# Kernel optimization log

Hardware: AMD Instinct MI355X
Metric: run time of the kernel (lower is better)

## Reference

```python
import jax, jax.numpy as jnp
import numpy as np

B, DC, DB, DF = 16384, 2048, 768, 256
NF = DB  # num_features (isSwinT=True)
EPS = 1e-5


def setup_inputs() -> dict:
    key = jax.random.key(0)
    ks = jax.random.split(key, 20)
    s = 0.02
    return {
        'x_context': jax.random.normal(ks[0], (B, DC), jnp.float32),
        'x_body': jax.random.normal(ks[1], (B, DB), jnp.float32),
        'x_face': jax.random.normal(ks[2], (B, DF), jnp.float32),
        'Wc': jax.random.normal(ks[3], (NF, DC), jnp.float32) * s,
        'bc': jax.random.normal(ks[4], (NF,), jnp.float32) * s,
        'Wa1': jax.random.normal(ks[5], (128, NF), jnp.float32) * s,
        'ba1': jax.random.normal(ks[6], (128,), jnp.float32) * s,
        'ga': jnp.ones((128,), jnp.float32),
        'bba': jnp.zeros((128,), jnp.float32),
        'Wa2': jax.random.normal(ks[7], (1, 128), jnp.float32) * s,
        'ba2': jax.random.normal(ks[8], (1,), jnp.float32) * s,
        'W1': jax.random.normal(ks[9], (256, NF * 3), jnp.float32) * s,
        'b1': jax.random.normal(ks[10], (256,), jnp.float32) * s,
        'g1': jnp.ones((256,), jnp.float32),
        'be1': jnp.zeros((256,), jnp.float32),
        'Wcat': jax.random.normal(ks[11], (26, 256), jnp.float32) * s,
        'bcat': jax.random.normal(ks[12], (26,), jnp.float32) * s,
    }


def _bn(x, g, b):
    # BatchNorm1d, training mode (biased batch stats), deterministic
    m = jnp.mean(x, axis=0)
    v = jnp.mean((x - m) ** 2, axis=0)
    return (x - m) * jax.lax.rsqrt(v + EPS) * g + b


def reference(x_context, x_body, x_face, Wc, bc, Wa1, ba1, ga, bba, Wa2, ba2,
              W1, b1, g1, be1, Wcat, bcat):
    # face repeated elementwise to body width: [B,256,1]->repeat(3)->view[B,768]
    face = jnp.repeat(x_face, DB // DF, axis=1)              # [B, NF]
    ctx = x_context @ Wc.T + bc                              # [B, NF]
    body = x_body                                            # [B, NF]

    def cross_atten(a, u, v):
        # two 1x1 dot-products, softmax over size-2 dim, weighted sum
        d = jnp.stack([jnp.sum(a * u, axis=1), jnp.sum(a * v, axis=1)], axis=1)  # [B,2]
        att = jax.nn.softmax(d, axis=1)
        # sum over dim2 of a[:, :, None] @ att[:, None, :] == a * att.sum(1)
        return a * jnp.sum(att, axis=1, keepdims=True)

    cfeat = cross_atten(ctx, body, face)
    bfeat = cross_atten(body, ctx, face)
    ffeat = cross_atten(face, ctx, body)

    def fc_att(x):
        h = _bn(x @ Wa1.T + ba1, ga, bba)
        h = jax.nn.gelu(h, approximate=False)
        return h @ Wa2.T + ba2                               # [B, 1]

    score = jax.nn.softmax(
        jnp.concatenate([fc_att(cfeat), fc_att(bfeat), fc_att(ffeat)], axis=1), axis=1)  # [B,3]
    cfeat = cfeat * score[:, 0:1]
    bfeat = bfeat * score[:, 1:2]
    ffeat = ffeat * score[:, 2:3]

    fuse = jnp.concatenate([cfeat, bfeat, ffeat], axis=1) @ W1.T + b1  # [B,256]
    fuse = jax.nn.relu(_bn(fuse, g1, be1))  # dropout p=0.5 treated as identity (eval)
    return fuse @ Wcat.T + bcat             # [B,26]
```

## Files before the change

### kernel.cpp

```cpp
#include <hip/hip_runtime.h>
#include <hip/hip_bf16.h>
#include <stdint.h>

typedef float f32x4 __attribute__((ext_vector_type(4)));
typedef short bf16x8 __attribute__((ext_vector_type(8)));
typedef unsigned short u16;

static constexpr int kB  = 16384;
static constexpr int kDC = 2048;
static constexpr int kNF = 768;
static constexpr float kEps = 1e-5f;

static constexpr size_t OFF_FEATS  = 0;
static constexpr size_t OFF_X      = 75497472;
static constexpr size_t OFF_WCBF   = OFF_X + 67108864;
static constexpr size_t OFF_WA1BF  = OFF_WCBF + 3145728;
static constexpr size_t OFF_W1BF   = OFF_WA1BF + 196608;
static constexpr size_t OFF_FUSE   = OFF_W1BF + 1179648;
static constexpr size_t OFF_SCORES = OFF_FUSE + 16777216;
static constexpr size_t OFF_STATS  = OFF_SCORES + 196608;

static __device__ __forceinline__ u16 f2bf(float x) {
  union { float f; unsigned u; } c; c.f = x;
  unsigned r = c.u + 0x7fffu + ((c.u >> 16) & 1u);
  return (u16)(r >> 16);
}

static __device__ __forceinline__ void cvt8x4(const float* __restrict__ in,
                                              u16* __restrict__ out, long base) {
  float4 f[8];
#pragma unroll
  for (int i = 0; i < 8; ++i) f[i] = ((const float4*)in)[base + i * 256];
#pragma unroll
  for (int i = 0; i < 8; ++i)
    ((ushort4*)out)[base + i * 256] =
        make_ushort4(f2bf(f[i].x), f2bf(f[i].y), f2bf(f[i].z), f2bf(f[i].w));
}

__global__ __launch_bounds__(256) void prep_kernel(
    const float* __restrict__ xc, const float* __restrict__ Wc,
    const float* __restrict__ Wa1, const float* __restrict__ W1,
    u16* __restrict__ axbf, u16* __restrict__ wcbf,
    u16* __restrict__ wa1bf, u16* __restrict__ w1bf)
{
  const int b = blockIdx.x, t = threadIdx.x;
  const float* in; u16* out; long base;
  if (b < 4096)      { in = xc;  out = axbf;  base = (long)b * 2048 + t; }
  else if (b < 4288) { in = Wc;  out = wcbf;  base = (long)(b - 4096) * 2048 + t; }
  else if (b < 4300) { in = Wa1; out = wa1bf; base = (long)(b - 4288) * 2048 + t; }
  else               { in = W1;  out = w1bf;  base = (long)(b - 4300) * 2048 + t; }
  cvt8x4(in, out, base);
}

static __device__ __forceinline__ void gload16(const void* g, void* l) {
  __builtin_amdgcn_global_load_lds(
      (const __attribute__((address_space(1))) void*)g,
      (__attribute__((address_space(3))) void*)l, 16, 0, 0);
}

__global__ __launch_bounds__(256) void gemm_ctx_conv(
    const u16* __restrict__ A, const u16* __restrict__ B,
    const float* __restrict__ bias, u16* __restrict__ C,
    const float* __restrict__ xb, const float* __restrict__ xf,
    u16* __restrict__ feats)
{
  __shared__ __align__(16) u16 As[128 * 32];
  __shared__ __align__(16) u16 Bs[128 * 32];
  const int id = blockIdx.x, t = threadIdx.x;

  if (id >= 768) {
    const int c = id - 768;
    if (c < 1536) {
      cvt8x4(xb, feats + (size_t)kB * kNF, (long)c * 2048 + t);
    } else {
      const long base = (long)(c - 1536) * 2048 + t;
      float4 f[8];
#pragma unroll
      for (int i = 0; i < 8; ++i) f[i] = ((const float4*)xf)[base + i * 256];
#pragma unroll
      for (int i = 0; i < 8; ++i) {
        const long v = base + i * 256;
        u16 e0 = f2bf(f[i].x), e1 = f2bf(f[i].y), e2 = f2bf(f[i].z), e3 = f2bf(f[i].w);
        size_t p = (size_t)v * 4;
        size_t row = p >> 8;
        int col = (int)(p & 255);
        u16* o = feats + (size_t)2 * kB * kNF + row * kNF + col * 3;
        ushort4* o4 = (ushort4*)o;
        o4[0] = make_ushort4(e0, e0, e0, e1);
        o4[1] = make_ushort4(e1, e1, e2, e2);
        o4[2] = make_ushort4(e2, e3, e3, e3);
      }
    }
    return;
  }

  const int bx = id & 127, by = id >> 7;
  const size_t m0 = (size_t)bx * 128;
  const int n0 = by * 128;
  const int lane = t & 63, wave = t >> 6;
  const int wm = (wave >> 1) * 64, wn = (wave & 1) * 64;
  const int fr = lane & 15, fq = lane >> 4;

  const int srow = t >> 2, scol = (t & 3) * 8;
  const u16* ga0 = A + (m0 + srow) * (size_t)kDC + scol;
  const u16* ga1 = A + (m0 + 64 + srow) * (size_t)kDC + scol;
  const u16* gb0 = B + (size_t)(n0 + srow) * kDC + scol;
  const u16* gb1 = B + (size_t)(n0 + 64 + srow) * kDC + scol;
  u16* la = As + t * 8;
  u16* lb = Bs + t * 8;
  const u16* fa = As + (wm + fr) * 32 + fq * 8;
  const u16* fb = Bs + (wn + fr) * 32 + fq * 8;

  f32x4 acc[4][4] = {};

  for (int k = 0; k < 64; ++k) {
    __syncthreads();
    gload16(ga0, la);
    gload16(ga1, la + 2048);
    gload16(gb0, lb);
    gload16(gb1, lb + 2048);
    ga0 += 32; ga1 += 32; gb0 += 32; gb1 += 32;
    __syncthreads();
    bf16x8 av[4], bv[4];
#pragma unroll
    for (int mf = 0; mf < 4; ++mf) av[mf] = *(const bf16x8*)(fa + mf * 512);
#pragma unroll
    for (int nf = 0; nf < 4; ++nf) bv[nf] = *(const bf16x8*)(fb + nf * 512);
#pragma unroll
    for (int mf = 0; mf < 4; ++mf)
#pragma unroll
      for (int nf = 0; nf < 4; ++nf)
        acc[mf][nf] = __builtin_amdgcn_mfma_f32_16x16x32_bf16(av[mf], bv[nf], acc[mf][nf], 0, 0, 0);
  }

#pragma unroll
  for (int mf = 0; mf < 4; ++mf) {
    const size_t rb = m0 + wm + mf * 16 + fq * 4;
#pragma unroll
    for (int nf = 0; nf < 4; ++nf) {
      const int gn = n0 + wn + nf * 16 + fr;
      const float bb = bias[gn];
#pragma unroll
      for (int rr = 0; rr < 4; ++rr)
        C[(rb + rr) * (size_t)kNF + gn] = f2bf(acc[mf][nf][rr] + bb);
    }
  }
}

template <int STATS>
__global__ __launch_bounds__(256) void gemm_bt64(
    const u16* __restrict__ A, int lda, const u16* __restrict__ B, int ldb,
    const float* __restrict__ bias, float* __restrict__ C, int ldc, int K,
    float* __restrict__ stats)
{
  __shared__ __align__(16) u16 As[2 * 64 * 32];
  __shared__ __align__(16) u16 Bs[2 * 128 * 32];
  const int bx = blockIdx.x, by = blockIdx.y;
  const size_t m0 = (size_t)bx * 64;
  const int n0 = by * 128;
  const int t = threadIdx.x;
  const int lane = t & 63, wave = t >> 6;
  const int wn = wave * 32;
  const int fr = lane & 15, fq = lane >> 4;

  const int srow = t >> 2, scol = (t & 3) * 8;
  const u16* ga0 = A + (m0 + srow) * (size_t)lda + scol;
  const u16* gb0 = B + (size_t)(n0 + srow) * ldb + scol;
  const u16* gb1 = B + (size_t)(n0 + 64 + srow) * ldb + scol;

  f32x4 acc[4][2] = {};

  gload16(ga0, As + t * 8);
  gload16(gb0, Bs + t * 8);
  gload16(gb1, Bs + t * 8 + 2048);
  ga0 += 32; gb0 += 32; gb1 += 32;
  __syncthreads();

  const int kt = K >> 5;
  for (int k = 0; k < kt; ++k) {
    const int cur = k & 1;
    if (k + 1 < kt) {
      u16* an = As + (cur ^ 1) * 2048;
      u16* bn = Bs + (cur ^ 1) * 4096;
      gload16(ga0, an + t * 8);
      gload16(gb0, bn + t * 8);
      gload16(gb1, bn + t * 8 + 2048);
      ga0 += 32; gb0 += 32; gb1 += 32;
    }
    const u16* fa = As + cur * 2048 + fr * 32 + fq * 8;
    const u16* fb = Bs + cur * 4096 + (wn + fr) * 32 + fq * 8;
    bf16x8 av[4], bv[2];
#pragma unroll
    for (int mf = 0; mf < 4; ++mf) av[mf] = *(const bf16x8*)(fa + mf * 512);
#pragma unroll
    for (int nf = 0; nf < 2; ++nf) bv[nf] = *(const bf16x8*)(fb + nf * 512);
#pragma unroll
    for (int mf = 0; mf < 4; ++mf)
#pragma unroll
      for (int nf = 0; nf < 2; ++nf)
        acc[mf][nf] = __builtin_amdgcn_mfma_f32_16x16x32_bf16(av[mf], bv[nf], acc[mf][nf], 0, 0, 0);
    __syncthreads();
  }

  float cs[2] = {}, cs2[2] = {};
#pragma unroll
  for (int mf = 0; mf < 4; ++mf) {
    const size_t rb = m0 + mf * 16 + fq * 4;
#pragma unroll
    for (int nf = 0; nf < 2; ++nf) {
      const int gn = n0 + wn + nf * 16 + fr;
      const float bb = bias[gn];
#pragma unroll
      for (int rr = 0; rr < 4; ++rr) {
        const float vv = acc[mf][nf][rr] + bb;
        C[(rb + rr) * (size_t)ldc + gn] = vv;
        if (STATS) { cs[nf] += vv; cs2[nf] += vv * vv; }
      }
    }
  }
  if (STATS) {
    const int f = (int)(m0 >> 14);
#pragma unroll
    for (int nf = 0; nf < 2; ++nf) {
      float s = cs[nf], s2 = cs2[nf];
      s += __shfl_down(s, 32); s2 += __shfl_down(s2, 32);
      s += __shfl_down(s, 16); s2 += __shfl_down(s2, 16);
      if (fq == 0) {
        const int gn = n0 + wn + nf * 16 + fr;
        atomicAdd(&stats[(f * 128 + gn) * 2 + 0], s);
        atomicAdd(&stats[(f * 128 + gn) * 2 + 1], s2);
      }
    }
  }
}

__global__ __launch_bounds__(256) void gemm_fuse64(
    const u16* __restrict__ feats, const u16* __restrict__ w1,
    const float* __restrict__ scores, const float* __restrict__ b1,
    float* __restrict__ fuse, float* __restrict__ fstats)
{
  __shared__ __align__(16) u16 As[2 * 64 * 32];
  __shared__ __align__(16) u16 Bs[2 * 128 * 32];
  const int bx = blockIdx.x, by = blockIdx.y;
  const size_t m0 = (size_t)bx * 64;
  const int n0 = by * 128;
  const int t = threadIdx.x;
  const int lane = t & 63, wave = t >> 6;
  const int wn = wave * 32;
  const int fr = lane & 15, fq = lane >> 4;
  const int srow = t >> 2, scol = (t & 3) * 8;

  const u16* ga0; const u16* gb0; const u16* gb1;
  auto setf = [&](int f) {
    ga0 = feats + (size_t)f * kB * kNF + (m0 + srow) * (size_t)kNF + scol;
    gb0 = w1 + f * kNF + (size_t)(n0 + srow) * 2304 + scol;
    gb1 = gb0 + (size_t)64 * 2304;
  };

  const f32x4 vzero = {};
  f32x4 acc[4][2] = {}, tot[4][2] = {};

  setf(0);
  gload16(ga0, As + t * 8);
  gload16(gb0, Bs + t * 8);
  gload16(gb1, Bs + t * 8 + 2048);
  ga0 += 32; gb0 += 32; gb1 += 32;
  int pf = 0, pk = 1;
  int ck = 0, cf = 0;
  __syncthreads();

  for (int s = 0; s < 72; ++s) {
    const int cur = s & 1;
    if (s < 71) {
      u16* an = As + (cur ^ 1) * 2048;
      u16* bn = Bs + (cur ^ 1) * 4096;
      gload16(ga0, an + t * 8);
      gload16(gb0, bn + t * 8);
      gload16(gb1, bn + t * 8 + 2048);
      if (++pk == 24) { pk = 0; ++pf; if (pf < 3) setf(pf); }
      else { ga0 += 32; gb0 += 32; gb1 += 32; }
    }
    const u16* fa = As + cur * 2048 + fr * 32 + fq * 8;
    const u16* fb = Bs + cur * 4096 + (wn + fr) * 32 + fq * 8;
    bf16x8 av[4], bv[2];
#pragma unroll
    for (int mf = 0; mf < 4; ++mf) av[mf] = *(const bf16x8*)(fa + mf * 512);
#pragma unroll
    for (int nf = 0; nf < 2; ++nf) bv[nf] = *(const bf16x8*)(fb + nf * 512);
#pragma unroll
    for (int mf = 0; mf < 4; ++mf)
#pragma unroll
      for (int nf = 0; nf < 2; ++nf)
        acc[mf][nf] = __builtin_amdgcn_mfma_f32_16x16x32_bf16(av[mf], bv[nf], acc[mf][nf], 0, 0, 0);
    if (++ck == 24) {
      ck = 0;
#pragma unroll
      for (int mf = 0; mf < 4; ++mf) {
        const size_t rb = m0 + mf * 16 + fq * 4;
#pragma unroll
        for (int rr = 0; rr < 4; ++rr) {
          const float sv = scores[(rb + rr) * 3 + cf];
#pragma unroll
          for (int nf = 0; nf < 2; ++nf) tot[mf][nf][rr] += sv * acc[mf][nf][rr];
        }
      }
#pragma unroll
      for (int mf = 0; mf < 4; ++mf)
#pragma unroll
        for (int nf = 0; nf < 2; ++nf) acc[mf][nf] = vzero;
      ++cf;
    }
    __syncthreads();
  }

  float cs[2] = {}, cs2[2] = {};
#pragma unroll
  for (int mf = 0; mf < 4; ++mf) {
    const size_t rb = m0 + mf * 16 + fq * 4;
#pragma unroll
    for (int nf = 0; nf < 2; ++nf) {
      const int gn = n0 + wn + nf * 16 + fr;
      const float bb = b1[gn];
#pragma unroll
      for (int rr = 0; rr < 4; ++rr) {
        const float vv = tot[mf][nf][rr] + bb;
        fuse[(rb + rr) * 256 + gn] = vv;
        cs[nf] += vv; cs2[nf] += vv * vv;
      }
    }
  }
#pragma unroll
  for (int nf = 0; nf < 2; ++nf) {
    float s = cs[nf], s2 = cs2[nf];
    s += __shfl_down(s, 32); s2 += __shfl_down(s2, 32);
    s += __shfl_down(s, 16); s2 += __shfl_down(s2, 16);
    if (fq == 0) {
      const int gn = n0 + wn + nf * 16 + fr;
      atomicAdd(&fstats[gn * 2 + 0], s);
      atomicAdd(&fstats[gn * 2 + 1], s2);
    }
  }
}

__global__ __launch_bounds__(64) void att_kernel(
    const float* __restrict__ H, const float* __restrict__ stats,
    const float* __restrict__ ga, const float* __restrict__ bba,
    const float* __restrict__ Wa2, const float* __restrict__ ba2,
    float* __restrict__ scores)
{
  const int i = blockIdx.x, l = threadIdx.x;
  float d[3];
#pragma unroll
  for (int f = 0; f < 3; ++f) {
    float part = 0.f;
#pragma unroll
    for (int h = 0; h < 2; ++h) {
      const int c = l + h * 64;
      const float sum = stats[(f * 128 + c) * 2 + 0];
      const float sq  = stats[(f * 128 + c) * 2 + 1];
      const float m = sum * (1.f / kB);
      const float var = sq * (1.f / kB) - m * m;
      const float rs = rsqrtf(var + kEps);
      const float x = H[((size_t)f * kB + i) * 128 + c];
      const float xn = (x - m) * rs * ga[c] + bba[c];
      const float ge = 0.5f * xn * (1.f + erff(xn * 0.70710678118f));
      part += ge * Wa2[c];
    }
#pragma unroll
    for (int off = 32; off > 0; off >>= 1) part += __shfl_down(part, off);
    d[f] = part;
  }
  if (l == 0) {
    const float b2 = ba2[0];
    float d0 = d[0] + b2, d1 = d[1] + b2, d2 = d[2] + b2;
    const float mx = fmaxf(d0, fmaxf(d1, d2));
    const float e0 = expf(d0 - mx), e1 = expf(d1 - mx), e2 = expf(d2 - mx);
    const float inv = 1.f / (e0 + e1 + e2);
    scores[i * 3 + 0] = e0 * inv;
    scores[i * 3 + 1] = e1 * inv;
    scores[i * 3 + 2] = e2 * inv;
  }
}

__global__ __launch_bounds__(64) void final_kernel(
    const float* __restrict__ fuse, const float* __restrict__ fstats,
    const float* __restrict__ g1, const float* __restrict__ be1,
    const float* __restrict__ Wcat, const float* __restrict__ bcat,
    float* __restrict__ out)
{
  const int i = blockIdx.x, l = threadIdx.x;
  __shared__ float row[256];
#pragma unroll
  for (int h = 0; h < 4; ++h) {
    const int c = l + h * 64;
    const float sum = fstats[c * 2 + 0], sq = fstats[c * 2 + 1];
    const float m = sum * (1.f / kB);
    const float var = sq * (1.f / kB) - m * m;
    const float rs = rsqrtf(var + kEps);
    const float v = (fuse[(size_t)i * 256 + c] - m) * rs * g1[c] + be1[c];
    row[c] = fmaxf(v, 0.f);
  }
  __syncthreads();
  if (l < 26) {
    float acc = bcat[l];
    const float* w = Wcat + l * 256;
    for (int k2 = 0; k2 < 256; ++k2) acc += row[k2] * w[k2];
    out[(size_t)i * 26 + l] = acc;
  }
}

extern "C" void kernel_launch(void* const* d_in, const int* in_sizes, int n_in,
                              void* d_out, int out_size, void* d_ws, size_t ws_size,
                              hipStream_t stream) {
  (void)in_sizes; (void)n_in; (void)out_size; (void)ws_size;
  const float* xc   = (const float*)d_in[0];
  const float* xb   = (const float*)d_in[1];
  const float* xf   = (const float*)d_in[2];
  const float* Wc   = (const float*)d_in[3];
  const float* bc   = (const float*)d_in[4];
  const float* Wa1  = (const float*)d_in[5];
  const float* ba1  = (const float*)d_in[6];
  const float* ga   = (const float*)d_in[7];
  const float* bba  = (const float*)d_in[8];
  const float* Wa2  = (const float*)d_in[9];
  const float* ba2  = (const float*)d_in[10];
  const float* W1   = (const float*)d_in[11];
  const float* b1   = (const float*)d_in[12];
  const float* g1   = (const float*)d_in[13];
  const float* be1  = (const float*)d_in[14];
  const float* Wcat = (const float*)d_in[15];
  const float* bcat = (const float*)d_in[16];
  float* out = (float*)d_out;

  char* ws = (char*)d_ws;
  u16* feats   = (u16*)(ws + OFF_FEATS);
  u16* axbf    = (u16*)(ws + OFF_X);
  float* H     = (float*)(ws + OFF_X);
  u16* wcbf    = (u16*)(ws + OFF_WCBF);
  u16* wa1bf   = (u16*)(ws + OFF_WA1BF);
  u16* w1bf    = (u16*)(ws + OFF_W1BF);
  float* fuse  = (float*)(ws + OFF_FUSE);
  float* scores= (float*)(ws + OFF_SCORES);
  float* hst   = (float*)(ws + OFF_STATS);
  float* fst   = (float*)(ws + OFF_STATS + 3072);

  hipMemsetAsync(ws + OFF_STATS, 0, 5120, stream);
  prep_kernel<<<4372, 256, 0, stream>>>(xc, Wc, Wa1, W1, axbf, wcbf, wa1bf, w1bf);
  gemm_ctx_conv<<<2816, 256, 0, stream>>>(axbf, wcbf, bc, feats, xb, xf, feats);
  gemm_bt64<1><<<dim3(768, 1), 256, 0, stream>>>(feats, kNF, wa1bf, kNF, ba1, H, 128, kNF, hst);
  att_kernel<<<kB, 64, 0, stream>>>(H, hst, ga, bba, Wa2, ba2, scores);
  gemm_fuse64<<<dim3(256, 2), 256, 0, stream>>>(feats, w1bf, scores, b1, fuse, fst);
  final_kernel<<<kB, 64, 0, stream>>>(fuse, fst, g1, be1, Wcat, bcat, out);
}
```

Before: 290.4 us.

## Fuse x_context bf16 conversion into context GEMM A-tile loading

Drops the separate pass that converts the 16384x2048 fp32 context input to bf16 in workspace. The context GEMM now reads fp32 A directly into registers, converts to bf16 and writes to LDS, with a one-step register prefetch of the next K slice. This removes a 128MB read plus 64MB write/read round trip, but the GEMM now reads fp32 A (twice the bytes) through registers instead of async global-to-LDS loads, and A is re-read by each of the 6 N-tile blocks.

```diff
diff --git a/kernel.cpp b/kernel.cpp
--- a/kernel.cpp
+++ b/kernel.cpp
@@ -26,6 +26,12 @@
   return (u16)(r >> 16);
 }
 
+static __device__ __forceinline__ unsigned pk2(float lo, float hi) {
+  union { __hip_bfloat162 h; unsigned u; } c;
+  c.h = __float22bfloat162_rn(make_float2(lo, hi));
+  return c.u;
+}
+
 static __device__ __forceinline__ void cvt8x4(const float* __restrict__ in,
                                               u16* __restrict__ out, long base) {
   float4 f[8];
@@ -37,18 +43,15 @@
         make_ushort4(f2bf(f[i].x), f2bf(f[i].y), f2bf(f[i].z), f2bf(f[i].w));
 }
 
-__global__ __launch_bounds__(256) void prep_kernel(
-    const float* __restrict__ xc, const float* __restrict__ Wc,
-    const float* __restrict__ Wa1, const float* __restrict__ W1,
-    u16* __restrict__ axbf, u16* __restrict__ wcbf,
-    u16* __restrict__ wa1bf, u16* __restrict__ w1bf)
+__global__ __launch_bounds__(256) void prep_w(
+    const float* __restrict__ Wc, const float* __restrict__ Wa1, const float* __restrict__ W1,
+    u16* __restrict__ wcbf, u16* __restrict__ wa1bf, u16* __restrict__ w1bf)
 {
   const int b = blockIdx.x, t = threadIdx.x;
   const float* in; u16* out; long base;
-  if (b < 4096)      { in = xc;  out = axbf;  base = (long)b * 2048 + t; }
-  else if (b < 4288) { in = Wc;  out = wcbf;  base = (long)(b - 4096) * 2048 + t; }
-  else if (b < 4300) { in = Wa1; out = wa1bf; base = (long)(b - 4288) * 2048 + t; }
-  else               { in = W1;  out = w1bf;  base = (long)(b - 4300) * 2048 + t; }
+  if (b < 192)      { in = Wc;  out = wcbf;  base = (long)b * 2048 + t; }
+  else if (b < 204) { in = Wa1; out = wa1bf; base = (long)(b - 192) * 2048 + t; }
+  else              { in = W1;  out = w1bf;  base = (long)(b - 204) * 2048 + t; }
   cvt8x4(in, out, base);
 }
 
@@ -58,8 +61,8 @@
       (__attribute__((address_space(3))) void*)l, 16, 0, 0);
 }
 
-__global__ __launch_bounds__(256) void gemm_ctx_conv(
-    const u16* __restrict__ A, const u16* __restrict__ B,
+__global__ __launch_bounds__(256) void gemm_mega(
+    const float* __restrict__ A, const u16* __restrict__ B,
     const float* __restrict__ bias, u16* __restrict__ C,
     const float* __restrict__ xb, const float* __restrict__ xf,
     u16* __restrict__ feats)
@@ -102,24 +105,41 @@
   const int fr = lane & 15, fq = lane >> 4;
 
   const int srow = t >> 2, scol = (t & 3) * 8;
-  const u16* ga0 = A + (m0 + srow) * (size_t)kDC + scol;
-  const u16* ga1 = A + (m0 + 64 + srow) * (size_t)kDC + scol;
   const u16* gb0 = B + (size_t)(n0 + srow) * kDC + scol;
   const u16* gb1 = B + (size_t)(n0 + 64 + srow) * kDC + scol;
-  u16* la = As + t * 8;
   u16* lb = Bs + t * 8;
+
+  const int arow = t >> 1, ah = (t & 1);
+  const float* ga = A + (m0 + arow) * (size_t)kDC + ah * 16;
+  u16* lawr = As + arow * 32 + ah * 16;
+
   const u16* fa = As + (wm + fr) * 32 + fq * 8;
   const u16* fb = Bs + (wn + fr) * 32 + fq * 8;
 
   f32x4 acc[4][4] = {};
-
+  float4 ra0, ra1, ra2, ra3;
+  auto loadA = [&]() {
+    ra0 = ((const float4*)ga)[0]; ra1 = ((const float4*)ga)[1];
+    ra2 = ((const float4*)ga)[2]; ra3 = ((const float4*)ga)[3];
+  };
+  auto cvtWrite = [&]() {
+    uint4 w0, w1;
+    w0.x = pk2(ra0.x, ra0.y); w0.y = pk2(ra0.z, ra0.w);
+    w0.z = pk2(ra1.x, ra1.y); w0.w = pk2(ra1.z, ra1.w);
+    w1.x = pk2(ra2.x, ra2.y); w1.y = pk2(ra2.z, ra2.w);
+    w1.z = pk2(ra3.x, ra3.y); w1.w = pk2(ra3.z, ra3.w);
+    ((uint4*)lawr)[0] = w0;
+    ((uint4*)(lawr + 8))[0] = w1;
+  };
+
+  loadA();
   for (int k = 0; k < 64; ++k) {
     __syncthreads();
-    gload16(ga0, la);
-    gload16(ga1, la + 2048);
     gload16(gb0, lb);
     gload16(gb1, lb + 2048);
-    ga0 += 32; ga1 += 32; gb0 += 32; gb1 += 32;
+    gb0 += 32; gb1 += 32;
+    cvtWrite();
+    if (k < 63) { ga += 32; loadA(); }
     __syncthreads();
     bf16x8 av[4], bv[4];
 #pragma unroll
@@ -434,7 +454,6 @@
 
   char* ws = (char*)d_ws;
   u16* feats   = (u16*)(ws + OFF_FEATS);
-  u16* axbf    = (u16*)(ws + OFF_X);
   float* H     = (float*)(ws + OFF_X);
   u16* wcbf    = (u16*)(ws + OFF_WCBF);
   u16* wa1bf   = (u16*)(ws + OFF_WA1BF);
@@ -445,8 +464,8 @@
   float* fst   = (float*)(ws + OFF_STATS + 3072);
 
   hipMemsetAsync(ws + OFF_STATS, 0, 5120, stream);
-  prep_kernel<<<4372, 256, 0, stream>>>(xc, Wc, Wa1, W1, axbf, wcbf, wa1bf, w1bf);
-  gemm_ctx_conv<<<2816, 256, 0, stream>>>(axbf, wcbf, bc, feats, xb, xf, feats);
+  prep_w<<<276, 256, 0, stream>>>(Wc, Wa1, W1, wcbf, wa1bf, w1bf);
+  gemm_mega<<<2816, 256, 0, stream>>>(xc, wcbf, bc, feats, xb, xf, feats);
   gemm_bt64<1><<<dim3(768, 1), 256, 0, stream>>>(feats, kNF, wa1bf, kNF, ba1, H, 128, kNF, hst);
   att_kernel<<<kB, 64, 0, stream>>>(H, hst, ga, bba, Wa2, ba2, scores);
   gemm_fuse64<<<dim3(256, 2), 256, 0, stream>>>(feats, w1bf, scores, b1, fuse, fst);
```

New measurement: 305.4 us. 5.2% more time.
